# Optimization experiments

Hardware: AMD Instinct MI355X
Metric: run time of the kernel (lower is better)

Reference implementation:

```python
import jax, jax.numpy as jnp
import numpy as np

B, T, C = 2, 2048, 2048
H, KH, D = 16, 4, 128
EPS = 1e-6

def _rmsnorm(x, w, eps=EPS):
    # norm over last dim in fp32, matching torch RMSNorm
    xf = x.astype(jnp.float32)
    var = jnp.mean(xf * xf, axis=-1, keepdims=True)
    return w * (xf * jax.lax.rsqrt(var + eps)).astype(x.dtype)

def _rotate_half(x):
    x1, x2 = jnp.split(x, 2, axis=-1)
    return jnp.concatenate((-x2, x1), axis=-1)

def setup_inputs() -> dict:
    key = jax.random.key(0)
    ks = jax.random.split(key, 9)
    s = 0.02
    return {
        "x": jax.random.normal(ks[0], (B, T, C), jnp.float32),
        "cos": jax.random.uniform(ks[1], (B, T, D), jnp.float32),
        "sin": jax.random.uniform(ks[2], (B, T, D), jnp.float32),
        "Wq": jax.random.normal(ks[3], (H * D, C), jnp.float32) * s,
        "Wk": jax.random.normal(ks[4], (KH * D, C), jnp.float32) * s,
        "Wv": jax.random.normal(ks[5], (KH * D, C), jnp.float32) * s,
        "Wo": jax.random.normal(ks[6], (C, H * D), jnp.float32) * s,
        "q_norm_w": jnp.ones((D,), jnp.float32),
        "k_norm_w": jnp.ones((D,), jnp.float32),
    }

def reference(x, cos, sin, Wq, Wk, Wv, Wo, q_norm_w, k_norm_w):
    rep = H // KH
    # projections (torch Linear: y = x @ W.T)
    q = jnp.einsum('btc,oc->bto', x, Wq).reshape(B, T, H, D)
    k = jnp.einsum('btc,oc->bto', x, Wk).reshape(B, T, KH, D)
    v = jnp.einsum('btc,oc->bto', x, Wv).reshape(B, T, KH, D)
    # per-head RMSNorm on d_head
    q = _rmsnorm(q, q_norm_w)
    k = _rmsnorm(k, k_norm_w)
    # RoPE, cos/sin broadcast over heads
    c = cos[:, :, None, :]
    s = sin[:, :, None, :]
    q = q * c + _rotate_half(q) * s
    k = k * c + _rotate_half(k) * s
    # GQA attention without materializing repeated k/v
    qg = q.reshape(B, T, KH, rep, D)
    scale = 1.0 / jnp.sqrt(jnp.asarray(D, jnp.float32))
    scores = jnp.einsum('bqhrd,bkhd->bhrqk', qg, k) * scale  # (B,KH,rep,T,T)
    causal = jnp.tril(jnp.ones((T, T), bool))
    scores = jnp.where(causal, scores, jnp.finfo(scores.dtype).min)
    attn = jax.nn.softmax(scores, axis=-1)
    y = jnp.einsum('bhrqk,bkhd->bqhrd', attn, v)  # (B,T,KH,rep,D)
    y = y.reshape(B, T, H * D)
    return jnp.einsum('bto,co->btc', y, Wo)
```

## Files before the change

kernel.cpp:

```cpp
#include <hip/hip_runtime.h>


typedef __attribute__((ext_vector_type(8))) short bf16x8;
typedef __attribute__((ext_vector_type(4))) float f32x4;
typedef __attribute__((ext_vector_type(16))) float f32x16;

__device__ __forceinline__ unsigned short f2bf(float f) {
  union { float f; unsigned u; } v; v.f = f;
  unsigned u = v.u;
  u += 0x7fffu + ((u >> 16) & 1u);
  return (unsigned short)(u >> 16);
}
__device__ __forceinline__ float bf2f(unsigned short h) {
  union { unsigned u; float f; } v; v.u = ((unsigned)h) << 16;
  return v.f;
}
__device__ __forceinline__ unsigned cvtpk_bf16(float lo, float hi) {
  unsigned r;
  asm("v_cvt_pk_bf16_f32 %0, %1, %2" : "=v"(r) : "v"(lo), "v"(hi));
  return r;
}

__device__ __forceinline__ void gl_lds16(const void* g, void* l) {
  __builtin_amdgcn_global_load_lds(
      (const __attribute__((address_space(1))) unsigned int*)(unsigned long long)g,
      (__attribute__((address_space(3))) unsigned int*)(unsigned int)(unsigned long long)l,
      16, 0, 0);
}

__global__ void cvt_all(const float* __restrict__ x, const float* __restrict__ wq,
                        const float* __restrict__ wk, const float* __restrict__ wv,
                        const float* __restrict__ wo,
                        unsigned short* __restrict__ xb,
                        unsigned short* __restrict__ wcat,
                        unsigned short* __restrict__ wob) {
  const long nx = 2097152, nq = 1048576, nk = 262144;
  const long b1 = nx, b2 = nx + nq, b3 = b2 + nk, b4 = b3 + nk;
  const long tot = b4 + 1048576;
  long i = (long)blockIdx.x * blockDim.x + threadIdx.x;
  const long stride = (long)gridDim.x * blockDim.x;
  for (; i < tot; i += stride) {
    float4 vv; unsigned short* dst; long o;
    if (i < b1)      { vv = ((const float4*)x)[i];       dst = xb;   o = i; }
    else if (i < b2) { vv = ((const float4*)wq)[i - b1]; dst = wcat; o = i - b1; }
    else if (i < b3) { vv = ((const float4*)wk)[i - b2]; dst = wcat; o = (i - b2) + nq; }
    else if (i < b4) { vv = ((const float4*)wv)[i - b3]; dst = wcat; o = (i - b3) + nq + nk; }
    else             { vv = ((const float4*)wo)[i - b4]; dst = wob;  o = i - b4; }
    ushort4 u;
    u.x = f2bf(vv.x); u.y = f2bf(vv.y); u.z = f2bf(vv.z); u.w = f2bf(vv.w);
    ((ushort4*)dst)[o] = u;
  }
}

#define PHASE(QM, QN, PF, GATE)                                               \
  {                                                                           \
    bf16x8 af[4][2], bg[2][2];                                                \
    _Pragma("unroll") for (int r = 0; r < 4; ++r) {                           \
      const char* pa = ldsc + curb + (((QM)*128 + arow0 + r*16) << 7);        \
      af[r][0] = *(const bf16x8*)(pa + csw0);                                 \
      af[r][1] = *(const bf16x8*)(pa + csw1);                                 \
    }                                                                         \
    _Pragma("unroll") for (int n = 0; n < 2; ++n) {                           \
      const char* pb = ldsc + curb + 32768 + (((QN)*128 + brow0 + n*16) << 7);\
      bg[n][0] = *(const bf16x8*)(pb + csw0);                                 \
      bg[n][1] = *(const bf16x8*)(pb + csw1);                                 \
    }                                                                         \
    PF                                                                        \
    __builtin_amdgcn_s_barrier();                                             \
    asm volatile("s_waitcnt lgkmcnt(0)" ::: "memory");                        \
    __builtin_amdgcn_sched_barrier(0);                                        \
    __builtin_amdgcn_s_setprio(1);                                            \
    _Pragma("unroll") for (int r = 0; r < 4; ++r)                             \
      _Pragma("unroll") for (int n = 0; n < 2; ++n) {                         \
        acc[(QM)*4+r][(QN)*2+n] = __builtin_amdgcn_mfma_f32_16x16x32_bf16(    \
            af[r][0], bg[n][0], acc[(QM)*4+r][(QN)*2+n], 0, 0, 0);            \
        acc[(QM)*4+r][(QN)*2+n] = __builtin_amdgcn_mfma_f32_16x16x32_bf16(    \
            af[r][1], bg[n][1], acc[(QM)*4+r][(QN)*2+n], 0, 0, 0);            \
      }                                                                       \
    __builtin_amdgcn_s_setprio(0);                                            \
    GATE                                                                      \
    __builtin_amdgcn_s_barrier();                                             \
  }

template <int OUT_BF16>
__global__ __launch_bounds__(512, 2)
void gemm256(const unsigned short* __restrict__ A,
             const unsigned short* __restrict__ Bm,
             void* __restrict__ Cp, int M, int N, int K) {
  __shared__ __align__(16) char ldsc[131072];
  const int nbn = N >> 8;
  int wg = blockIdx.x;
  {
    const int cpx = (int)gridDim.x >> 3;
    wg = (wg & 7) * cpx + (wg >> 3);
  }
  const int m0 = (wg / nbn) << 8, n0 = (wg % nbn) << 8;
  const int tid = threadIdx.x;
  const int lane = tid & 63, wid = tid >> 6;
  const int lr = lane & 15, lg = lane >> 4;
  const int wm = wid >> 2, wn = wid & 3;
  const int csw0 = (lg << 4) ^ ((lr & 7) << 4);
  const int csw1 = (64 + (lg << 4)) ^ ((lr & 7) << 4);
  const int arow0 = (wm << 6) + lr;
  const int brow0 = (wn << 5) + lr;
  const int srowL = tid >> 3;
  const int scol = ((tid & 7) ^ (srowL & 7)) << 3;
  const unsigned short* Asrc = A + (size_t)(m0 + srowL) * K + scol;
  const unsigned short* Bsrc = Bm + (size_t)(n0 + srowL) * K + scol;
  const int sdst = wid << 10;
  const int NT = K >> 6;
  f32x4 acc[8][4] = {};
  gl_lds16(Asrc, ldsc + sdst);
  gl_lds16(Asrc + (size_t)64 * K, ldsc + 8192 + sdst);
  gl_lds16(Bsrc, ldsc + 32768 + sdst);
  gl_lds16(Bsrc + (size_t)64 * K, ldsc + 40960 + sdst);
  gl_lds16(Asrc + (size_t)128 * K, ldsc + 16384 + sdst);
  gl_lds16(Asrc + (size_t)192 * K, ldsc + 24576 + sdst);
  gl_lds16(Bsrc + (size_t)128 * K, ldsc + 49152 + sdst);
  gl_lds16(Bsrc + (size_t)192 * K, ldsc + 57344 + sdst);
  asm volatile("s_waitcnt vmcnt(4)" ::: "memory");
  __builtin_amdgcn_s_barrier();

  for (int t = 0; t < NT; ++t) {
    const int curb = (t & 1) << 16;
    const int nxtb = curb ^ 65536;
    const size_t kn = (size_t)(t + 1) << 6;
    const bool pf = (t + 1) < NT;
    PHASE(0, 0,
      if (pf) { gl_lds16(Asrc + kn, ldsc + nxtb + sdst);
                gl_lds16(Asrc + (size_t)64 * K + kn, ldsc + nxtb + 8192 + sdst); },
      if (pf) { asm volatile("s_waitcnt vmcnt(2)" ::: "memory"); }
      else    { asm volatile("s_waitcnt vmcnt(0)" ::: "memory"); } )
    PHASE(1, 0,
      if (pf) { gl_lds16(Bsrc + kn, ldsc + nxtb + 32768 + sdst);
                gl_lds16(Bsrc + (size_t)64 * K + kn, ldsc + nxtb + 40960 + sdst); }, )
    PHASE(0, 1,
      if (pf) { gl_lds16(Asrc + (size_t)128 * K + kn, ldsc + nxtb + 16384 + sdst);
                gl_lds16(Asrc + (size_t)192 * K + kn, ldsc + nxtb + 24576 + sdst); }, )
    PHASE(1, 1,
      if (pf) { gl_lds16(Bsrc + (size_t)128 * K + kn, ldsc + nxtb + 49152 + sdst);
                gl_lds16(Bsrc + (size_t)192 * K + kn, ldsc + nxtb + 57344 + sdst); },
      if (pf) { asm volatile("s_waitcnt vmcnt(4)" ::: "memory"); } )
  }
  #pragma unroll
  for (int mi = 0; mi < 8; ++mi) {
    const int mrow = m0 + ((mi >> 2) << 7) + (wm << 6) + ((mi & 3) << 4) + (lg << 2);
    #pragma unroll
    for (int ni = 0; ni < 4; ++ni) {
      const int ncol = n0 + ((ni >> 1) << 7) + (wn << 5) + ((ni & 1) << 4) + lr;
      #pragma unroll
      for (int i = 0; i < 4; ++i) {
        if constexpr (OUT_BF16)
          ((unsigned short*)Cp)[(size_t)(mrow + i) * N + ncol] = f2bf(acc[mi][ni][i]);
        else
          ((float*)Cp)[(size_t)(mrow + i) * N + ncol] = acc[mi][ni][i];
      }
    }
  }
}

__global__ __launch_bounds__(512, 2)
void gemm128n(const unsigned short* __restrict__ A,
              const unsigned short* __restrict__ Bm,
              float* __restrict__ Cp, int M, int N, int K) {
  __shared__ __align__(16) char ldsc[98304];
  const int nbn = N >> 8;
  int wg = blockIdx.x;
  { const int cpx = (int)gridDim.x >> 3;
    wg = (wg & 7) * cpx + (wg >> 3); }
  const int m0 = (wg / nbn) << 7, n0 = (wg % nbn) << 8;
  const int tid = threadIdx.x;
  const int lane = tid & 63, wid = tid >> 6;
  const int lr = lane & 15, lg = lane >> 4;
  const int wm = wid >> 1, wn = wid & 1;
  const int csw0 = (lg << 4) ^ ((lr & 7) << 4);
  const int csw1 = (64 + (lg << 4)) ^ ((lr & 7) << 4);
  const int srowL = tid >> 3;
  const int scol = ((tid & 7) ^ (srowL & 7)) << 3;
  const unsigned short* Asrc = A + (size_t)(m0 + srowL) * K + scol;
  const unsigned short* Bsrc = Bm + (size_t)(n0 + srowL) * K + scol;
  const int sdst = wid << 10;
  const int NT = K >> 6;
  f32x4 acc[2][8] = {};
  gl_lds16(Asrc, ldsc + sdst);
  gl_lds16(Asrc + (size_t)64 * K, ldsc + 8192 + sdst);
  gl_lds16(Bsrc, ldsc + 16384 + sdst);
  gl_lds16(Bsrc + (size_t)128 * K, ldsc + 24576 + sdst);
  gl_lds16(Bsrc + (size_t)64 * K, ldsc + 32768 + sdst);
  gl_lds16(Bsrc + (size_t)192 * K, ldsc + 40960 + sdst);
  asm volatile("s_waitcnt vmcnt(2)" ::: "memory");
  __builtin_amdgcn_s_barrier();

  for (int t = 0; t < NT; ++t) {
    const int curb = (t & 1) ? 49152 : 0;
    const int nxtb = 49152 - curb;
    const size_t kn = (size_t)(t + 1) << 6;
    const bool pf = (t + 1) < NT;
    #pragma unroll
    for (int ph = 0; ph < 2; ++ph) {
      bf16x8 af[2][2], bg[4][2];
      #pragma unroll
      for (int r = 0; r < 2; ++r) {
        const char* pa = ldsc + curb + (((wm << 5) + (r << 4) + lr) << 7);
        af[r][0] = *(const bf16x8*)(pa + csw0);
        af[r][1] = *(const bf16x8*)(pa + csw1);
      }
      #pragma unroll
      for (int n = 0; n < 4; ++n) {
        const char* pb = ldsc + curb + 16384 + ((ph << 1) + wn) * 8192 +
                         (((n << 4) + lr) << 7);
        bg[n][0] = *(const bf16x8*)(pb + csw0);
        bg[n][1] = *(const bf16x8*)(pb + csw1);
      }
      if (pf) {
        if (ph == 0) {
          gl_lds16(Asrc + kn, ldsc + nxtb + sdst);
          gl_lds16(Asrc + (size_t)64 * K + kn, ldsc + nxtb + 8192 + sdst);
          gl_lds16(Bsrc + kn, ldsc + nxtb + 16384 + sdst);
          gl_lds16(Bsrc + (size_t)128 * K + kn, ldsc + nxtb + 24576 + sdst);
        } else {
          gl_lds16(Bsrc + (size_t)64 * K + kn, ldsc + nxtb + 32768 + sdst);
          gl_lds16(Bsrc + (size_t)192 * K + kn, ldsc + nxtb + 40960 + sdst);
        }
      }
      __builtin_amdgcn_s_barrier();
      asm volatile("s_waitcnt lgkmcnt(0)" ::: "memory");
      __builtin_amdgcn_sched_barrier(0);
      __builtin_amdgcn_s_setprio(1);
      #pragma unroll
      for (int r = 0; r < 2; ++r)
        #pragma unroll
        for (int n = 0; n < 4; ++n) {
          acc[r][ph * 4 + n] = __builtin_amdgcn_mfma_f32_16x16x32_bf16(
              af[r][0], bg[n][0], acc[r][ph * 4 + n], 0, 0, 0);
          acc[r][ph * 4 + n] = __builtin_amdgcn_mfma_f32_16x16x32_bf16(
              af[r][1], bg[n][1], acc[r][ph * 4 + n], 0, 0, 0);
        }
      __builtin_amdgcn_s_setprio(0);
      if (ph == 0) {
        if (pf) { asm volatile("s_waitcnt vmcnt(4)" ::: "memory"); }
        else    { asm volatile("s_waitcnt vmcnt(0)" ::: "memory"); }
      } else {
        if (pf) { asm volatile("s_waitcnt vmcnt(2)" ::: "memory"); }
      }
      __builtin_amdgcn_s_barrier();
    }
  }
  #pragma unroll
  for (int r = 0; r < 2; ++r) {
    const int mrow = m0 + (wm << 5) + (r << 4) + (lg << 2);
    #pragma unroll
    for (int n = 0; n < 8; ++n) {
      const int ncol = n0 + (wn << 7) + (n << 4) + lr;
      #pragma unroll
      for (int i = 0; i < 4; ++i)
        Cp[(size_t)(mrow + i) * N + ncol] = acc[r][n][i];
    }
  }
}

__global__ __launch_bounds__(256)
void norm_rope(const unsigned short* __restrict__ qkv,
               const float* __restrict__ cosb, const float* __restrict__ sinb,
               const float* __restrict__ qw, const float* __restrict__ kw,
               unsigned short* __restrict__ Qb,
               unsigned short* __restrict__ Kb) {
  const int wv = threadIdx.x >> 6, l = threadIdx.x & 63;
  const int rr = blockIdx.x * 4 + wv;
  const int hh = rr % 20, bt = rr / 20;
  const bool isq = hh < 16;
  const ushort2 u = *(const ushort2*)(qkv + (size_t)bt * 3072 + (hh << 7) + 2 * l);
  const float v0 = bf2f(u.x), v1 = bf2f(u.y);
  float ss = v0 * v0 + v1 * v1;
  #pragma unroll
  for (int off = 1; off < 64; off <<= 1) ss += __shfl_xor(ss, off);
  const float rms = rsqrtf(ss * (1.0f / 128.0f) + 1e-6f);
  const float* w = isq ? qw : kw;
  const float2 w2 = *(const float2*)(w + 2 * l);
  const float n0 = v0 * rms * w2.x, n1 = v1 * rms * w2.y;
  const float sx0 = __shfl_xor(n0, 32), sx1 = __shfl_xor(n1, 32);
  const float p0 = (l < 32) ? -sx0 : sx0;
  const float p1 = (l < 32) ? -sx1 : sx1;
  const float2 c2 = *(const float2*)(cosb + (size_t)bt * 128 + 2 * l);
  const float2 s2 = *(const float2*)(sinb + (size_t)bt * 128 + 2 * l);
  const float qsc = isq ? 0.08838834764831845f : 1.0f;
  ushort2 o;
  o.x = f2bf((n0 * c2.x + p0 * s2.x) * qsc);
  o.y = f2bf((n1 * c2.y + p1 * s2.y) * qsc);
  const int b = bt >> 11, t = bt & 2047;
  if (isq)
    *(ushort2*)(Qb + (((size_t)(b * 16 + hh) * 2048 + t) << 7) + 2 * l) = o;
  else
    *(ushort2*)(Kb + (((size_t)(b * 4 + (hh - 16)) * 2048 + t) << 7) + 2 * l) = o;
}

__global__ __launch_bounds__(256)
void v_trans(const unsigned short* __restrict__ qkv, unsigned short* __restrict__ Vt) {
  __shared__ unsigned short tile[64][66];
  const int b = blockIdx.x >> 2, h = blockIdx.x & 3;
  const int t0 = blockIdx.y << 6, d0 = blockIdx.z << 6;
  const int tid = threadIdx.x;
  #pragma unroll
  for (int p = 0; p < 16; ++p) {
    const int id = (p << 8) + tid;
    const int r = id >> 6, c = id & 63;
    tile[r][c] = qkv[(size_t)(b * 2048 + t0 + r) * 3072 + 2560 + (h << 7) + d0 + c];
  }
  __syncthreads();
  #pragma unroll
  for (int p = 0; p < 16; ++p) {
    const int id = (p << 8) + tid;
    const int r = id >> 6, c = id & 63;
    const int cp = (c & 48) | ((c & 8) >> 1) | ((c & 4) << 1) | (c & 3);
    Vt[(size_t)((b * 4 + h) * 128 + d0 + r) * 2048 + t0 + cp] = tile[c][r];
  }
}

__global__ __launch_bounds__(512)
void attn_fwd(const unsigned short* __restrict__ Qb,
              const unsigned short* __restrict__ Kb,
              const unsigned short* __restrict__ Vt,
              unsigned short* __restrict__ Y) {
  __shared__ __align__(16) char L[65536];
  const int bh = blockIdx.x;
  const int b = bh >> 4, h = bh & 15, hk = h >> 2;
  const int p = blockIdx.y;
  const int tid = threadIdx.x;
  const int lane = tid & 63, wid = tid >> 6;
  const int g = wid >> 2;
  const int wid2 = wid & 3;
  const int j = wid2 >> 1;
  const int qt = j ? (31 - p) : p;
  const int sub = (wid2 & 1) << 5;
  const int l31 = lane & 31, hi = lane >> 5;
  const int swb = (lane & 7) << 4;
  char* KsC = L + g * 32768;
  char* VsC = KsC + 16384;
  const unsigned short* Kp = Kb + (size_t)(b * 4 + hk) * 2048 * 128;
  const unsigned short* Vp = Vt + (size_t)(b * 4 + hk) * 128 * 2048;
  const int qg = qt * 64 + sub + l31;
  const unsigned short* Qp = Qb + (size_t)((b * 16 + h) * 2048 + qg) * 128;
  bf16x8 aq[8];
  #pragma unroll
  for (int ks = 0; ks < 8; ++ks)
    aq[ks] = *(const bf16x8*)(Qp + (ks << 4) + (hi << 3));
  float m_i = -1e30f, l_i = 0.f;
  f32x16 acc[4] = {};
  const int kr_in = (lane >> 4), kcb = (lane & 15) << 4;
  const int vr_in = (lane >> 3), vcb = (lane & 7) << 4;
  const int nkb = 32 - p;
  const int nit = (nkb + 1) >> 1;

  for (int it = 0; it < nit; ++it) {
    const int kb = 2 * it + g;
    const bool act = kb < nkb;
    if (act) {
      const int k0 = kb << 6;
      #pragma unroll
      for (int i = 0; i < 4; ++i) {
        const int c = (wid2 << 2) + i;
        { const int r = (c << 2) + kr_in;
          const int sw = kcb ^ ((r & 7) << 4);
          gl_lds16(Kp + (size_t)(k0 + r) * 128 + (sw >> 1), KsC + (c << 10)); }
        { const int r = (c << 3) + vr_in;
          const int sw = vcb ^ ((r & 7) << 4);
          gl_lds16(Vp + (size_t)r * 2048 + k0 + (sw >> 1), VsC + (c << 10)); }
      }
    }
    __syncthreads();
    if (act && kb <= qt) {
      const int k0 = kb << 6;
      f32x16 s[2] = {};
      __builtin_amdgcn_s_setprio(1);
      #pragma unroll
      for (int sblk = 0; sblk < 2; ++sblk) {
        const int row = (sblk << 5) + l31;
        #pragma unroll
        for (int ks = 0; ks < 8; ++ks) {
          const bf16x8 bk = *(const bf16x8*)(
              KsC + (row << 8) + (((ks << 5) + (hi << 4)) ^ swb));
          s[sblk] = __builtin_amdgcn_mfma_f32_32x32x16_bf16(bk, aq[ks], s[sblk], 0, 0, 0);
        }
      }
      __builtin_amdgcn_s_setprio(0);
      if (kb == qt) {
        #pragma unroll
        for (int sblk = 0; sblk < 2; ++sblk)
          #pragma unroll
          for (int r = 0; r < 16; ++r) {
            const int kv = k0 + (sblk << 5) + (r & 3) + ((r >> 2) << 3) + (hi << 2);
            if (kv > qg) s[sblk][r] = -1e30f;
          }
      }
      float mx = s[0][0];
      #pragma unroll
      for (int sblk = 0; sblk < 2; ++sblk)
        #pragma unroll
        for (int r = 0; r < 16; ++r) mx = fmaxf(mx, s[sblk][r]);
      mx = fmaxf(mx, __shfl_xor(mx, 32));
      if (!__all(mx <= m_i + 8.0f)) {
        const float mn = fmaxf(m_i, mx);
        const float r = __expf(m_i - mn);
        m_i = mn;
        l_i *= r;
        #pragma unroll
        for (int d = 0; d < 4; ++d)
          #pragma unroll
          for (int i = 0; i < 16; ++i) acc[d][i] *= r;
      }
      float se = 0.f;
      unsigned pk[16];
      #pragma unroll
      for (int t2 = 0; t2 < 16; ++t2) {
        const int f0 = 2 * t2, f1 = 2 * t2 + 1;
        const float e0 = __expf(s[f0 >> 4][f0 & 15] - m_i);
        const float e1 = __expf(s[f1 >> 4][f1 & 15] - m_i);
        se += e0 + e1;
        pk[t2] = cvtpk_bf16(e0, e1);
      }
      se += __shfl_xor(se, 32);
      l_i += se;
      __builtin_amdgcn_s_setprio(1);
      #pragma unroll
      for (int dblk = 0; dblk < 4; ++dblk) {
        const int row = (dblk << 5) + l31;
        #pragma unroll
        for (int cp = 0; cp < 4; ++cp) {
          const bf16x8 va = *(const bf16x8*)(
              VsC + (row << 7) + (((cp << 5) + (hi << 4)) ^ swb));
          union { unsigned u[4]; bf16x8 v; } pb;
          pb.u[0] = pk[cp * 4 + 0]; pb.u[1] = pk[cp * 4 + 1];
          pb.u[2] = pk[cp * 4 + 2]; pb.u[3] = pk[cp * 4 + 3];
          acc[dblk] = __builtin_amdgcn_mfma_f32_32x32x16_bf16(va, pb.v, acc[dblk], 0, 0, 0);
        }
      }
      __builtin_amdgcn_s_setprio(0);
    }
    __syncthreads();
  }

  float* cb = (float*)L;
  #pragma unroll
  for (int jj = 0; jj < 2; ++jj) {
    const int base = (((wid2 & 1) << 6) + lane) * 66;
    if (g == 1 && j == jj) {
      #pragma unroll
      for (int d = 0; d < 4; ++d)
        #pragma unroll
        for (int i = 0; i < 16; ++i) cb[base + d * 16 + i] = acc[d][i];
      cb[base + 64] = m_i;
      cb[base + 65] = l_i;
    }
    __syncthreads();
    if (g == 0 && j == jj) {
      const float m1 = cb[base + 64], l1v = cb[base + 65];
      const float m = fmaxf(m_i, m1);
      const float e0 = __expf(m_i - m), e1 = __expf(m1 - m);
      const float inv = 1.0f / (l_i * e0 + l1v * e1);
      unsigned short* Yp = Y + (((size_t)b * 2048 + qg) * 16 + h) * 128;
      #pragma unroll
      for (int dblk = 0; dblk < 4; ++dblk) {
        #pragma unroll
        for (int qd = 0; qd < 4; ++qd) {
          ushort4 o;
          o.x = f2bf((acc[dblk][qd * 4 + 0] * e0 + cb[base + dblk * 16 + qd * 4 + 0] * e1) * inv);
          o.y = f2bf((acc[dblk][qd * 4 + 1] * e0 + cb[base + dblk * 16 + qd * 4 + 1] * e1) * inv);
          o.z = f2bf((acc[dblk][qd * 4 + 2] * e0 + cb[base + dblk * 16 + qd * 4 + 2] * e1) * inv);
          o.w = f2bf((acc[dblk][qd * 4 + 3] * e0 + cb[base + dblk * 16 + qd * 4 + 3] * e1) * inv);
          *(ushort4*)(Yp + (dblk << 5) + (qd << 3) + (hi << 2)) = o;
        }
      }
    }
    __syncthreads();
  }
}

extern "C" void kernel_launch(void* const* d_in, const int* in_sizes, int n_in,
                              void* d_out, int out_size, void* d_ws, size_t ws_size,
                              hipStream_t stream) {
  const float* x    = (const float*)d_in[0];
  const float* cosb = (const float*)d_in[1];
  const float* sinb = (const float*)d_in[2];
  const float* Wq   = (const float*)d_in[3];
  const float* Wk   = (const float*)d_in[4];
  const float* Wv   = (const float*)d_in[5];
  const float* Wo   = (const float*)d_in[6];
  const float* qw   = (const float*)d_in[7];
  const float* kw   = (const float*)d_in[8];
  char* ws = (char*)d_ws;
  unsigned short* xb   = (unsigned short*)(ws);
  unsigned short* Wcat = (unsigned short*)(ws + (16ull << 20));
  unsigned short* Wob  = (unsigned short*)(ws + (28ull << 20));
  unsigned short* qkv  = (unsigned short*)(ws + (36ull << 20));
  unsigned short* Qb   = (unsigned short*)(ws + (60ull << 20));
  unsigned short* Kb   = (unsigned short*)(ws + (76ull << 20));
  unsigned short* Vt   = (unsigned short*)(ws + (80ull << 20));

  cvt_all<<<2048, 256, 0, stream>>>(x, Wq, Wk, Wv, Wo, xb, Wcat, Wob);

  gemm256<1><<<192, 512, 0, stream>>>(xb, Wcat, qkv, 4096, 3072, 2048);
  norm_rope<<<2 * 2048 * 20 / 4, 256, 0, stream>>>(qkv, cosb, sinb, qw, kw, Qb, Kb);
  v_trans<<<dim3(8, 32, 2), 256, 0, stream>>>(qkv, Vt);
  attn_fwd<<<dim3(32, 16), 512, 0, stream>>>(Qb, Kb, Vt, xb);
  gemm128n<<<256, 512, 0, stream>>>(xb, Wob, (float*)d_out, 4096, 2048, 2048);
}
```

Before: 230.6 us.

## Fuse RMSNorm, RoPE and V transpose into QKV GEMM epilogue

The QKV projection GEMM now stages its bf16 output tile in LDS and applies per-head RMSNorm plus RoPE (for Q/K column blocks) or transposes V into the attention layout directly in the epilogue. This removes the intermediate qkv buffer round-trip and two separate kernel launches (norm_rope and v_trans). In exchange, the GEMM epilogue becomes longer with extra LDS traffic, barriers and scattered global reads of cos/sin, which may lengthen the tail of the 192-block GEMM.

```diff
diff --git a/kernel.cpp b/kernel.cpp
--- a/kernel.cpp
+++ b/kernel.cpp
@@ -82,11 +82,15 @@
     __builtin_amdgcn_s_barrier();                                             \
   }
 
-template <int OUT_BF16>
 __global__ __launch_bounds__(512, 2)
-void gemm256(const unsigned short* __restrict__ A,
-             const unsigned short* __restrict__ Bm,
-             void* __restrict__ Cp, int M, int N, int K) {
+void gemm_qkv(const unsigned short* __restrict__ A,
+              const unsigned short* __restrict__ Bm,
+              const float* __restrict__ cosb, const float* __restrict__ sinb,
+              const float* __restrict__ qw, const float* __restrict__ kw,
+              unsigned short* __restrict__ Qb,
+              unsigned short* __restrict__ Kb,
+              unsigned short* __restrict__ Vt,
+              int M, int N, int K) {
   __shared__ __align__(16) char ldsc[131072];
   const int nbn = N >> 8;
   int wg = blockIdx.x;
@@ -142,20 +146,105 @@
                 gl_lds16(Bsrc + (size_t)192 * K + kn, ldsc + nxtb + 57344 + sdst); },
       if (pf) { asm volatile("s_waitcnt vmcnt(4)" ::: "memory"); } )
   }
-  #pragma unroll
-  for (int mi = 0; mi < 8; ++mi) {
-    const int mrow = m0 + ((mi >> 2) << 7) + (wm << 6) + ((mi & 3) << 4) + (lg << 2);
+
+  unsigned short (*vt)[138] = (unsigned short (*)[138])ldsc;
+  float* ssq = (float*)(ldsc + 70656);
+  const int nb = wg % nbn;
+  const int kind = (nb < 8) ? 0 : (nb < 10 ? 1 : 2);
+
+  for (int hsel = 0; hsel < 2; ++hsel) {
     #pragma unroll
-    for (int ni = 0; ni < 4; ++ni) {
-      const int ncol = n0 + ((ni >> 1) << 7) + (wn << 5) + ((ni & 1) << 4) + lr;
-      #pragma unroll
-      for (int i = 0; i < 4; ++i) {
-        if constexpr (OUT_BF16)
-          ((unsigned short*)Cp)[(size_t)(mrow + i) * N + ncol] = f2bf(acc[mi][ni][i]);
-        else
-          ((float*)Cp)[(size_t)(mrow + i) * N + ncol] = acc[mi][ni][i];
-      }
-    }
+    for (int mi = 0; mi < 8; ++mi) {
+      const int rl = ((mi >> 2) << 7) + (wm << 6) + ((mi & 3) << 4) + (lg << 2);
+      f32x4 cs = {};
+      #pragma unroll
+      for (int nih = 0; nih < 2; ++nih) {
+        const int ni = (hsel << 1) + nih;
+        const int ch = (wn << 5) + (nih << 4) + lr;
+        #pragma unroll
+        for (int i = 0; i < 4; ++i) {
+          const float v = acc[mi][ni][i];
+          vt[rl + i][ch] = f2bf(v);
+          cs[i] += v * v;
+        }
+      }
+      if (kind < 2) {
+        #pragma unroll
+        for (int off = 1; off < 16; off <<= 1) {
+          cs[0] += __shfl_xor(cs[0], off);
+          cs[1] += __shfl_xor(cs[1], off);
+          cs[2] += __shfl_xor(cs[2], off);
+          cs[3] += __shfl_xor(cs[3], off);
+        }
+        if (lr == 0) {
+          float* sp = ssq + (wn << 8) + rl;
+          sp[0] = cs[0]; sp[1] = cs[1]; sp[2] = cs[2]; sp[3] = cs[3];
+        }
+      }
+    }
+    __syncthreads();
+
+    if (kind < 2) {
+      const int r = tid >> 1, hf = tid & 1;
+      const int bt = m0 + r;
+      const float ssum = ssq[r] + ssq[256 + r] + ssq[512 + r] + ssq[768 + r];
+      const float rms = rsqrtf(ssum * 0.0078125f + 1e-6f);
+      const int hh = ((kind == 0 ? n0 : n0 - 2048) >> 7) + hsel;
+      const float* wv = (kind == 0) ? qw : kw;
+      const float qsc = (kind == 0) ? 0.08838834764831845f : 1.0f;
+      unsigned short* outp = (kind == 0)
+          ? Qb + ((((size_t)(bt >> 11) * 16 + hh) * 2048 + (bt & 2047)) << 7)
+          : Kb + ((((size_t)(bt >> 11) * 4 + hh) * 2048 + (bt & 2047)) << 7);
+      const float sgn = hf ? 1.0f : -1.0f;
+      #pragma unroll
+      for (int c8 = 0; c8 < 64; c8 += 8) {
+        const int c = (hf << 6) + c8;
+        const int cp = c ^ 64;
+        const float4 cv0 = *(const float4*)(cosb + (size_t)bt * 128 + c);
+        const float4 cv1 = *(const float4*)(cosb + (size_t)bt * 128 + c + 4);
+        const float4 sv0 = *(const float4*)(sinb + (size_t)bt * 128 + c);
+        const float4 sv1 = *(const float4*)(sinb + (size_t)bt * 128 + c + 4);
+        const float4 wv0 = *(const float4*)(wv + c);
+        const float4 wv1 = *(const float4*)(wv + c + 4);
+        const float4 wp0 = *(const float4*)(wv + cp);
+        const float4 wp1 = *(const float4*)(wv + cp + 4);
+        float o[8];
+        #pragma unroll
+        for (int j = 0; j < 8; ++j) {
+          const float wj  = (j < 4) ? ((const float*)&wv0)[j] : ((const float*)&wv1)[j - 4];
+          const float wpj = (j < 4) ? ((const float*)&wp0)[j] : ((const float*)&wp1)[j - 4];
+          const float cj  = (j < 4) ? ((const float*)&cv0)[j] : ((const float*)&cv1)[j - 4];
+          const float sj  = (j < 4) ? ((const float*)&sv0)[j] : ((const float*)&sv1)[j - 4];
+          const float nv = bf2f(vt[r][c + j]) * rms * wj;
+          const float pv = bf2f(vt[r][cp + j]) * rms * wpj;
+          o[j] = (nv * cj + sgn * pv * sj) * qsc;
+        }
+        ushort4 u0, u1;
+        u0.x = f2bf(o[0]); u0.y = f2bf(o[1]); u0.z = f2bf(o[2]); u0.w = f2bf(o[3]);
+        u1.x = f2bf(o[4]); u1.y = f2bf(o[5]); u1.z = f2bf(o[6]); u1.w = f2bf(o[7]);
+        *(ushort4*)(outp + c) = u0;
+        *(ushort4*)(outp + c + 4) = u1;
+      }
+    } else {
+      const int hk = ((n0 - 2560) >> 7) + hsel;
+      const int o4 = lane << 2;
+      const int blk = o4 & 192;
+      const int gg = (o4 >> 2) & 15;
+      const int ggp = (gg & 12) | ((gg & 1) << 1) | ((gg & 2) >> 1);
+      const int tin = blk + (ggp << 2);
+      unsigned short* vbase = Vt + (((size_t)(m0 >> 11) * 4 + hk) << 18) + (m0 & 2047);
+      #pragma unroll
+      for (int dd = 0; dd < 16; ++dd) {
+        const int d = (wid << 4) + dd;
+        ushort4 u;
+        u.x = vt[tin + 0][d];
+        u.y = vt[tin + 1][d];
+        u.z = vt[tin + 2][d];
+        u.w = vt[tin + 3][d];
+        *(ushort4*)(vbase + ((size_t)d << 11) + o4) = u;
+      }
+    }
+    __syncthreads();
   }
 }
 
@@ -256,63 +345,6 @@
       for (int i = 0; i < 4; ++i)
         Cp[(size_t)(mrow + i) * N + ncol] = acc[r][n][i];
     }
-  }
-}
-
-__global__ __launch_bounds__(256)
-void norm_rope(const unsigned short* __restrict__ qkv,
-               const float* __restrict__ cosb, const float* __restrict__ sinb,
-               const float* __restrict__ qw, const float* __restrict__ kw,
-               unsigned short* __restrict__ Qb,
-               unsigned short* __restrict__ Kb) {
-  const int wv = threadIdx.x >> 6, l = threadIdx.x & 63;
-  const int rr = blockIdx.x * 4 + wv;
-  const int hh = rr % 20, bt = rr / 20;
-  const bool isq = hh < 16;
-  const ushort2 u = *(const ushort2*)(qkv + (size_t)bt * 3072 + (hh << 7) + 2 * l);
-  const float v0 = bf2f(u.x), v1 = bf2f(u.y);
-  float ss = v0 * v0 + v1 * v1;
-  #pragma unroll
-  for (int off = 1; off < 64; off <<= 1) ss += __shfl_xor(ss, off);
-  const float rms = rsqrtf(ss * (1.0f / 128.0f) + 1e-6f);
-  const float* w = isq ? qw : kw;
-  const float2 w2 = *(const float2*)(w + 2 * l);
-  const float n0 = v0 * rms * w2.x, n1 = v1 * rms * w2.y;
-  const float sx0 = __shfl_xor(n0, 32), sx1 = __shfl_xor(n1, 32);
-  const float p0 = (l < 32) ? -sx0 : sx0;
-  const float p1 = (l < 32) ? -sx1 : sx1;
-  const float2 c2 = *(const float2*)(cosb + (size_t)bt * 128 + 2 * l);
-  const float2 s2 = *(const float2*)(sinb + (size_t)bt * 128 + 2 * l);
-  const float qsc = isq ? 0.08838834764831845f : 1.0f;
-  ushort2 o;
-  o.x = f2bf((n0 * c2.x + p0 * s2.x) * qsc);
-  o.y = f2bf((n1 * c2.y + p1 * s2.y) * qsc);
-  const int b = bt >> 11, t = bt & 2047;
-  if (isq)
-    *(ushort2*)(Qb + (((size_t)(b * 16 + hh) * 2048 + t) << 7) + 2 * l) = o;
-  else
-    *(ushort2*)(Kb + (((size_t)(b * 4 + (hh - 16)) * 2048 + t) << 7) + 2 * l) = o;
-}
-
-__global__ __launch_bounds__(256)
-void v_trans(const unsigned short* __restrict__ qkv, unsigned short* __restrict__ Vt) {
-  __shared__ unsigned short tile[64][66];
-  const int b = blockIdx.x >> 2, h = blockIdx.x & 3;
-  const int t0 = blockIdx.y << 6, d0 = blockIdx.z << 6;
-  const int tid = threadIdx.x;
-  #pragma unroll
-  for (int p = 0; p < 16; ++p) {
-    const int id = (p << 8) + tid;
-    const int r = id >> 6, c = id & 63;
-    tile[r][c] = qkv[(size_t)(b * 2048 + t0 + r) * 3072 + 2560 + (h << 7) + d0 + c];
-  }
-  __syncthreads();
-  #pragma unroll
-  for (int p = 0; p < 16; ++p) {
-    const int id = (p << 8) + tid;
-    const int r = id >> 6, c = id & 63;
-    const int cp = (c & 48) | ((c & 8) >> 1) | ((c & 4) << 1) | (c & 3);
-    Vt[(size_t)((b * 4 + h) * 128 + d0 + r) * 2048 + t0 + cp] = tile[c][r];
   }
 }
 
@@ -491,16 +523,14 @@
   unsigned short* xb   = (unsigned short*)(ws);
   unsigned short* Wcat = (unsigned short*)(ws + (16ull << 20));
   unsigned short* Wob  = (unsigned short*)(ws + (28ull << 20));
-  unsigned short* qkv  = (unsigned short*)(ws + (36ull << 20));
-  unsigned short* Qb   = (unsigned short*)(ws + (60ull << 20));
-  unsigned short* Kb   = (unsigned short*)(ws + (76ull << 20));
-  unsigned short* Vt   = (unsigned short*)(ws + (80ull << 20));
+  unsigned short* Qb   = (unsigned short*)(ws + (36ull << 20));
+  unsigned short* Kb   = (unsigned short*)(ws + (52ull << 20));
+  unsigned short* Vt   = (unsigned short*)(ws + (56ull << 20));
 
   cvt_all<<<2048, 256, 0, stream>>>(x, Wq, Wk, Wv, Wo, xb, Wcat, Wob);
 
-  gemm256<1><<<192, 512, 0, stream>>>(xb, Wcat, qkv, 4096, 3072, 2048);
-  norm_rope<<<2 * 2048 * 20 / 4, 256, 0, stream>>>(qkv, cosb, sinb, qw, kw, Qb, Kb);
-  v_trans<<<dim3(8, 32, 2), 256, 0, stream>>>(qkv, Vt);
+  gemm_qkv<<<192, 512, 0, stream>>>(xb, Wcat, cosb, sinb, qw, kw,
+                                    Qb, Kb, Vt, 4096, 3072, 2048);
   attn_fwd<<<dim3(32, 16), 512, 0, stream>>>(Qb, Kb, Vt, xb);
   gemm128n<<<256, 512, 0, stream>>>(xb, Wob, (float*)d_out, 4096, 2048, 2048);
 }
```

Result: slower. 263.2 us (+14.2%).
